# Kernel optimization log

Hardware: AMD Instinct MI355X
Metric: run time of the kernel (lower is better)

Reference implementation:

```python
import jax, jax.numpy as jnp
import numpy as np

N = 100000      # number of 1-simplices (edges of the power grid)
NNZ = 3200000   # nonzeros in L1_tilde (avg degree 32)
CIN = 128
COUT = 128
BN_EPS = 1e-5


def setup_inputs() -> dict:
    key = jax.random.key(0)
    ks = jax.random.split(key, 8)
    Z_H = jax.random.normal(ks[0], (N, CIN), dtype=jnp.float32)
    rows = jax.random.randint(ks[1], (NNZ,), 0, N)
    cols = jax.random.randint(ks[2], (NNZ,), 0, N)
    values = jax.random.normal(ks[3], (NNZ,), dtype=jnp.float32)
    # nn.Linear params (Kaiming-ish scale)
    W = jax.random.normal(ks[4], (CIN, COUT), dtype=jnp.float32) / np.float32(np.sqrt(CIN))
    b = jnp.zeros((COUT,), dtype=jnp.float32)
    # BatchNorm1d affine params
    gamma = jnp.ones((COUT,), dtype=jnp.float32)
    beta = jnp.zeros((COUT,), dtype=jnp.float32)
    return {"Z_H": Z_H, "values": values, "W": W, "b": b,
            "gamma": gamma, "beta": beta, "rows": rows, "cols": cols}


def reference(Z_H, values, W, b, gamma, beta, rows, cols):
    # Linear projection: [N, CIN] @ [CIN, COUT] + [COUT]
    Z_theta = Z_H @ W + b
    # Sparse Laplacian matmul (COO SpMM): Z_conv[r] += v * Z_theta[c]
    gathered = values[:, None] * Z_theta[cols]          # [NNZ, COUT]
    Z_conv = jax.ops.segment_sum(gathered, rows, num_segments=Z_H.shape[0])
    # BatchNorm1d (training mode: biased batch stats over the node dim)
    mean = jnp.mean(Z_conv, axis=0)
    var = jnp.var(Z_conv, axis=0)
    Z_bn = (Z_conv - mean) * (gamma / jnp.sqrt(var + BN_EPS)) + beta
    # ReLU + row-wise max pool -> [N, 1]
    Z_psi = jax.nn.relu(Z_bn)
    return jnp.max(Z_psi, axis=1, keepdims=True)
```

## Files before the change

### kernel.cpp

```cpp
#include <hip/hip_runtime.h>
#include <hip/hip_bf16.h>

#define CIN  128
#define COUT 128
#define BN_EPS 1e-5f
#define RPB   64
#define MAXNB 2048
#define PCHUNK 8192
#define CAP   2560
#define LDP   136

typedef __attribute__((ext_vector_type(8))) short short8;
typedef __attribute__((ext_vector_type(4))) float f32x4;

__device__ __forceinline__ unsigned pk2bf(float lo, float hi) {
    union { __hip_bfloat162 h; unsigned u; } c;
    c.h = __float22bfloat162_rn(make_float2(lo, hi));
    return c.u;
}

__device__ __forceinline__ unsigned short f2bf(float f) {
    unsigned u = __float_as_uint(f);
    u += 0x7fffu + ((u >> 16) & 1u);
    return (unsigned short)(u >> 16);
}

__device__ __forceinline__ void gemm_body(
    const float* __restrict__ Z, const float* __restrict__ W,
    const float* __restrict__ b, unsigned short* __restrict__ Zt,
    int N, int bid, int gb)
{
    __shared__ unsigned short cls[64 * LDP];

    const int t    = threadIdx.x;
    const int lane = t & 63;
    const int wid  = t >> 6;
    const int lm   = lane & 15;
    const int lg   = lane >> 4;

    short8 bfr[4][8];
#pragma unroll
    for (int kc = 0; kc < 4; ++kc) {
#pragma unroll
        for (int ct = 0; ct < 8; ++ct) {
            union { short8 v; unsigned u32[4]; } bf;
#pragma unroll
            for (int e = 0; e < 8; e += 2) {
                const float w0 = W[(kc * 32 + lg * 8 + e)     * COUT + ct * 16 + lm];
                const float w1 = W[(kc * 32 + lg * 8 + e + 1) * COUT + ct * 16 + lm];
                bf.u32[e >> 1] = pk2bf(w0, w1);
            }
            bfr[kc][ct] = bf.v;
        }
    }

    float bias[8];
#pragma unroll
    for (int ct = 0; ct < 8; ++ct) bias[ct] = b[ct * 16 + lm];

    const int tr = t >> 4;
    const int cc = t & 15;

    const int ntiles = (N + 63) / 64;
    for (int tile = bid; tile < ntiles; tile += gb) {
        const int row0 = tile * 64 + wid * 16;
        const int arow = row0 + lm;
        const bool aval = arow < N;
        const float* zrow = Z + (size_t)arow * CIN;

        f32x4 acc[8];
#pragma unroll
        for (int ct = 0; ct < 8; ++ct) {
            f32x4 a = {bias[ct], bias[ct], bias[ct], bias[ct]};
            acc[ct] = a;
        }

#pragma unroll
        for (int kc = 0; kc < 4; ++kc) {
            union { short8 v; unsigned u32[4]; } af;
            if (aval) {
                const float4 z0 = *((const float4*)(zrow + kc * 32 + lg * 8));
                const float4 z1 = *((const float4*)(zrow + kc * 32 + lg * 8 + 4));
                af.u32[0] = pk2bf(z0.x, z0.y);
                af.u32[1] = pk2bf(z0.z, z0.w);
                af.u32[2] = pk2bf(z1.x, z1.y);
                af.u32[3] = pk2bf(z1.z, z1.w);
            } else {
#pragma unroll
                for (int e = 0; e < 4; ++e) af.u32[e] = 0;
            }
#pragma unroll
            for (int ct = 0; ct < 8; ++ct)
                acc[ct] = __builtin_amdgcn_mfma_f32_16x16x32_bf16(
                    af.v, bfr[kc][ct], acc[ct], 0, 0, 0);
        }

        __syncthreads();
#pragma unroll
        for (int i = 0; i < 4; ++i) {
            const int r = wid * 16 + lg * 4 + i;
#pragma unroll
            for (int ct = 0; ct < 8; ct += 2) {
                const unsigned u = pk2bf(acc[ct][i], acc[ct + 1][i]);
                cls[r * LDP + ct * 16 + lm]       = (unsigned short)(u & 0xffffu);
                cls[r * LDP + (ct + 1) * 16 + lm] = (unsigned short)(u >> 16);
            }
        }
        __syncthreads();

#pragma unroll
        for (int j = 0; j < 4; ++j) {
            const int r = j * 16 + tr;
            const int grow = tile * 64 + r;
            if (grow < N) {
                const uint4 v = *((const uint4*)&cls[r * LDP + cc * 8]);
                *((uint4*)(Zt + (size_t)grow * COUT + cc * 8)) = v;
            }
        }
    }
}

__device__ __forceinline__ void partition_body(
    const int* __restrict__ rows, const int* __restrict__ cols,
    const float* __restrict__ vals, int* __restrict__ bucketCur,
    uint2* __restrict__ ebuck, int nnz, int NB, int pb)
{
    __shared__ int h[MAXNB];
    __shared__ int basecur[MAXNB];
    const int t = threadIdx.x;

    for (int i = t; i < NB; i += 256) h[i] = 0;
    __syncthreads();

    const int c0 = pb * PCHUNK;
    const int ce = min(c0 + PCHUNK, nnz);

    int rloc[PCHUNK / 256];
#pragma unroll
    for (int j = 0; j < PCHUNK / 256; ++j) {
        const int i = c0 + j * 256 + t;
        int r = -1;
        if (i < ce) r = rows[i];
        rloc[j] = r;
        if (r >= 0) atomicAdd(&h[r >> 6], 1);
    }
    __syncthreads();

    for (int i = t; i < NB; i += 256) {
        const int c = h[i];
        basecur[i] = c ? (i * CAP + atomicAdd(&bucketCur[i], c)) : 0;
    }
    __syncthreads();

#pragma unroll
    for (int j = 0; j < PCHUNK / 256; ++j) {
        const int i = c0 + j * 256 + t;
        const int r = rloc[j];
        if (r >= 0) {
            const int p = atomicAdd(&basecur[r >> 6], 1);
            ebuck[p] = make_uint2((unsigned)cols[i] | ((unsigned)(r & (RPB - 1)) << 17),
                                  __float_as_uint(vals[i]));
        }
    }
}

__global__ __launch_bounds__(256, 2) void gemm_part_kernel(
    const float* __restrict__ Z, const float* __restrict__ W,
    const float* __restrict__ b, unsigned short* __restrict__ Zt,
    const int* __restrict__ rows, const int* __restrict__ cols,
    const float* __restrict__ vals, int* __restrict__ bucketCur,
    uint2* __restrict__ ebuck, int nnz, int N, int NB, int pblocks, int gb)
{
    if ((int)blockIdx.x < pblocks) {
        partition_body(rows, cols, vals, bucketCur, ebuck, nnz, NB, blockIdx.x);
    } else {
        gemm_body(Z, W, b, Zt, N, blockIdx.x - pblocks, gb);
    }
}

__global__ __launch_bounds__(256) void gather_build_kernel(
    const unsigned short* __restrict__ Zt, const uint2* __restrict__ ebuck,
    const int* __restrict__ bucketCur, unsigned int* __restrict__ Zc,
    float* __restrict__ stats, int N)
{
    __shared__ int cnt[RPB];
    __shared__ int scn[RPB];
    __shared__ int loc[RPB];
    __shared__ uint2 ebuf[CAP];
    __shared__ float sbuf[256];

    const int t = threadIdx.x;
    const int b = blockIdx.x;
    const int base = b * CAP;
    int count = bucketCur[b];
    if (count > CAP) count = CAP;

    sbuf[t] = 0.f;
    if (t < RPB) cnt[t] = 0;
    __syncthreads();

    uint2 er[CAP / 256];
#pragma unroll
    for (int j = 0; j < CAP / 256; ++j) {
        const int i = j * 256 + t;
        if (i < count) {
            er[j] = ebuck[base + i];
            atomicAdd(&cnt[er[j].x >> 17], 1);
        }
    }
    __syncthreads();

    if (t < RPB) scn[t] = cnt[t];
    __syncthreads();
#pragma unroll
    for (int off = 1; off < RPB; off <<= 1) {
        int v = 0;
        if (t < RPB && t >= off) v = scn[t - off];
        __syncthreads();
        if (t < RPB) scn[t] += v;
        __syncthreads();
    }
    if (t < RPB) loc[t] = scn[t] - cnt[t];
    __syncthreads();

#pragma unroll
    for (int j = 0; j < CAP / 256; ++j) {
        const int i = j * 256 + t;
        if (i < count) {
            const uint2 e = er[j];
            const int rl  = (int)(e.x >> 17);
            const int pos = atomicAdd(&loc[rl], 1);
            ebuf[pos] = make_uint2(e.x & 0x1FFFFu, e.y);
        }
    }
    __syncthreads();

    const int wid  = t >> 6;
    const int lane = t & 63;
    const int eo   = lane >> 5;
    const int cg   = lane & 31;

    float s0 = 0.f, s1 = 0.f, s2 = 0.f, s3 = 0.f;
    float q0 = 0.f, q1 = 0.f, q2 = 0.f, q3 = 0.f;

    const int row0 = b * RPB;
    for (int r = wid; r < RPB; r += 4) {
        const int row = row0 + r;
        if (row >= N) break;
        const int end = scn[r];
        const int beg = end - cnt[r];

        float a0 = 0.f, a1 = 0.f, a2 = 0.f, a3 = 0.f;

        int i = beg + eo;
        for (; i + 6 < end; i += 8) {
            const uint2 p0 = ebuf[i];
            const uint2 p1 = ebuf[i + 2];
            const uint2 p2 = ebuf[i + 4];
            const uint2 p3 = ebuf[i + 6];
            const uint2 g0 = *((const uint2*)(Zt + (size_t)p0.x * COUT + cg * 4));
            const uint2 g1 = *((const uint2*)(Zt + (size_t)p1.x * COUT + cg * 4));
            const uint2 g2 = *((const uint2*)(Zt + (size_t)p2.x * COUT + cg * 4));
            const uint2 g3 = *((const uint2*)(Zt + (size_t)p3.x * COUT + cg * 4));
            const float v0 = __uint_as_float(p0.y);
            const float v1 = __uint_as_float(p1.y);
            const float v2 = __uint_as_float(p2.y);
            const float v3 = __uint_as_float(p3.y);
            a0 = fmaf(v0, __uint_as_float(g0.x << 16), a0);
            a1 = fmaf(v0, __uint_as_float(g0.x & 0xffff0000u), a1);
            a2 = fmaf(v0, __uint_as_float(g0.y << 16), a2);
            a3 = fmaf(v0, __uint_as_float(g0.y & 0xffff0000u), a3);
            a0 = fmaf(v1, __uint_as_float(g1.x << 16), a0);
            a1 = fmaf(v1, __uint_as_float(g1.x & 0xffff0000u), a1);
            a2 = fmaf(v1, __uint_as_float(g1.y << 16), a2);
            a3 = fmaf(v1, __uint_as_float(g1.y & 0xffff0000u), a3);
            a0 = fmaf(v2, __uint_as_float(g2.x << 16), a0);
            a1 = fmaf(v2, __uint_as_float(g2.x & 0xffff0000u), a1);
            a2 = fmaf(v2, __uint_as_float(g2.y << 16), a2);
            a3 = fmaf(v2, __uint_as_float(g2.y & 0xffff0000u), a3);
            a0 = fmaf(v3, __uint_as_float(g3.x << 16), a0);
            a1 = fmaf(v3, __uint_as_float(g3.x & 0xffff0000u), a1);
            a2 = fmaf(v3, __uint_as_float(g3.y << 16), a2);
            a3 = fmaf(v3, __uint_as_float(g3.y & 0xffff0000u), a3);
        }
        for (; i < end; i += 2) {
            const uint2 p = ebuf[i];
            const uint2 g = *((const uint2*)(Zt + (size_t)p.x * COUT + cg * 4));
            const float vp = __uint_as_float(p.y);
            a0 = fmaf(vp, __uint_as_float(g.x << 16), a0);
            a1 = fmaf(vp, __uint_as_float(g.x & 0xffff0000u), a1);
            a2 = fmaf(vp, __uint_as_float(g.y << 16), a2);
            a3 = fmaf(vp, __uint_as_float(g.y & 0xffff0000u), a3);
        }

        a0 += __shfl_xor(a0, 32);
        a1 += __shfl_xor(a1, 32);
        a2 += __shfl_xor(a2, 32);
        a3 += __shfl_xor(a3, 32);

        if (eo == 0) {
            uint2 o;
            o.x = pk2bf(a0, a1);
            o.y = pk2bf(a2, a3);
            *((uint2*)(Zc + (size_t)row * (COUT / 2) + cg * 2)) = o;
            s0 += a0; s1 += a1; s2 += a2; s3 += a3;
            q0 = fmaf(a0, a0, q0);
            q1 = fmaf(a1, a1, q1);
            q2 = fmaf(a2, a2, q2);
            q3 = fmaf(a3, a3, q3);
        }
    }

    if (eo == 0) {
        const int c0 = cg * 4;
        atomicAdd(&sbuf[c0 + 0], s0);
        atomicAdd(&sbuf[c0 + 1], s1);
        atomicAdd(&sbuf[c0 + 2], s2);
        atomicAdd(&sbuf[c0 + 3], s3);
        atomicAdd(&sbuf[128 + c0 + 0], q0);
        atomicAdd(&sbuf[128 + c0 + 1], q1);
        atomicAdd(&sbuf[128 + c0 + 2], q2);
        atomicAdd(&sbuf[128 + c0 + 3], q3);
    }
    __syncthreads();
    atomicAdd(&stats[t], sbuf[t]);
}

__global__ __launch_bounds__(256) void finalize_kernel(
    const unsigned int* __restrict__ Zc, const float* __restrict__ stats,
    const float* __restrict__ gamma, const float* __restrict__ beta,
    float* __restrict__ out, int N)
{
    const int row = blockIdx.x * 4 + (threadIdx.x >> 6);
    if (row >= N) return;
    const int lane = threadIdx.x & 63;
    const int c0 = lane * 2;

    const unsigned g = Zc[(size_t)row * (COUT / 2) + lane];
    const float x0 = __uint_as_float(g << 16);
    const float x1 = __uint_as_float(g & 0xffff0000u);

    const float invN = 1.0f / (float)N;
    const float m0 = stats[c0] * invN;
    const float m1 = stats[c0 + 1] * invN;
    const float v0 = stats[128 + c0] * invN - m0 * m0;
    const float v1 = stats[128 + c0 + 1] * invN - m1 * m1;
    const float sc0 = gamma[c0]     * rsqrtf(v0 + BN_EPS);
    const float sc1 = gamma[c0 + 1] * rsqrtf(v1 + BN_EPS);

    float y0 = (x0 - m0) * sc0 + beta[c0];
    float y1 = (x1 - m1) * sc1 + beta[c0 + 1];
    y0 = fmaxf(y0, 0.f);
    y1 = fmaxf(y1, 0.f);

    float mx = fmaxf(y0, y1);
#pragma unroll
    for (int off = 32; off > 0; off >>= 1)
        mx = fmaxf(mx, __shfl_xor(mx, off));

    if (lane == 0) out[row] = mx;
}

extern "C" void kernel_launch(void* const* d_in, const int* in_sizes, int n_in,
                              void* d_out, int out_size, void* d_ws, size_t ws_size,
                              hipStream_t stream)
{
    const float* Z_H   = (const float*)d_in[0];
    const float* vals  = (const float*)d_in[1];
    const float* W     = (const float*)d_in[2];
    const float* b     = (const float*)d_in[3];
    const float* gamma = (const float*)d_in[4];
    const float* beta  = (const float*)d_in[5];
    const int*   rows  = (const int*)d_in[6];
    const int*   cols  = (const int*)d_in[7];
    float* out = (float*)d_out;

    const int N   = in_sizes[0] / CIN;
    const int nnz = in_sizes[1];
    const int NB  = (N + RPB - 1) / RPB;
    const int pblocks = (nnz + PCHUNK - 1) / PCHUNK;
    const int ntiles  = (N + 63) / 64;
    const int gb      = (ntiles + 2) / 3;

    char* ws = (char*)d_ws;
    size_t off = 0;
    unsigned short* Zt = (unsigned short*)(ws + off); off += (size_t)N * COUT * sizeof(unsigned short);
    unsigned int*   Zc = (unsigned int*)(ws + off);   off += (size_t)N * (COUT / 2) * sizeof(unsigned int);
    uint2* ebuck  = (uint2*)(ws + off);  off += (size_t)NB * CAP * sizeof(uint2);
    int* bucketCur = (int*)(ws + off);   off += (size_t)NB * sizeof(int);
    float* stats   = (float*)(ws + off); off += 256 * sizeof(float);

    hipMemsetAsync(bucketCur, 0, ((size_t)NB + 256) * sizeof(int), stream);

    gemm_part_kernel<<<pblocks + gb, 256, 0, stream>>>(
        Z_H, W, b, Zt, rows, cols, vals, bucketCur, ebuck, nnz, N, NB, pblocks, gb);

    gather_build_kernel<<<NB, 256, 0, stream>>>(Zt, ebuck, bucketCur, Zc, stats, N);

    finalize_kernel<<<(N + 3) / 4, 256, 0, stream>>>(Zc, stats, gamma, beta, out, N);
}
```

Before: 242.9 us.

## Split SpMM gather into two 64-channel passes to halve per-pass row footprint

The SpMM aggregation loop now runs twice per block, each pass gathering only 64 of the 128 bf16 channels (4-byte loads instead of 8-byte) and writing half of each output row. Each pass touches a smaller slice of the gathered Z_theta rows, which may improve cache hit rates for the random gathers. In exchange, the edge list in shared memory is walked twice, the number of gather instructions doubles, and each load is narrower. The unused f2bf helper is also removed.

```diff
diff --git a/kernel.cpp b/kernel.cpp
--- a/kernel.cpp
+++ b/kernel.cpp
@@ -17,12 +17,6 @@
     union { __hip_bfloat162 h; unsigned u; } c;
     c.h = __float22bfloat162_rn(make_float2(lo, hi));
     return c.u;
-}
-
-__device__ __forceinline__ unsigned short f2bf(float f) {
-    unsigned u = __float_as_uint(f);
-    u += 0x7fffu + ((u >> 16) & 1u);
-    return (unsigned short)(u >> 16);
 }
 
 __device__ __forceinline__ void gemm_body(
@@ -240,87 +234,70 @@
     const int eo   = lane >> 5;
     const int cg   = lane & 31;
 
-    float s0 = 0.f, s1 = 0.f, s2 = 0.f, s3 = 0.f;
-    float q0 = 0.f, q1 = 0.f, q2 = 0.f, q3 = 0.f;
-
     const int row0 = b * RPB;
-    for (int r = wid; r < RPB; r += 4) {
-        const int row = row0 + r;
-        if (row >= N) break;
-        const int end = scn[r];
-        const int beg = end - cnt[r];
-
-        float a0 = 0.f, a1 = 0.f, a2 = 0.f, a3 = 0.f;
-
-        int i = beg + eo;
-        for (; i + 6 < end; i += 8) {
-            const uint2 p0 = ebuf[i];
-            const uint2 p1 = ebuf[i + 2];
-            const uint2 p2 = ebuf[i + 4];
-            const uint2 p3 = ebuf[i + 6];
-            const uint2 g0 = *((const uint2*)(Zt + (size_t)p0.x * COUT + cg * 4));
-            const uint2 g1 = *((const uint2*)(Zt + (size_t)p1.x * COUT + cg * 4));
-            const uint2 g2 = *((const uint2*)(Zt + (size_t)p2.x * COUT + cg * 4));
-            const uint2 g3 = *((const uint2*)(Zt + (size_t)p3.x * COUT + cg * 4));
-            const float v0 = __uint_as_float(p0.y);
-            const float v1 = __uint_as_float(p1.y);
-            const float v2 = __uint_as_float(p2.y);
-            const float v3 = __uint_as_float(p3.y);
-            a0 = fmaf(v0, __uint_as_float(g0.x << 16), a0);
-            a1 = fmaf(v0, __uint_as_float(g0.x & 0xffff0000u), a1);
-            a2 = fmaf(v0, __uint_as_float(g0.y << 16), a2);
-            a3 = fmaf(v0, __uint_as_float(g0.y & 0xffff0000u), a3);
-            a0 = fmaf(v1, __uint_as_float(g1.x << 16), a0);
-            a1 = fmaf(v1, __uint_as_float(g1.x & 0xffff0000u), a1);
-            a2 = fmaf(v1, __uint_as_float(g1.y << 16), a2);
-            a3 = fmaf(v1, __uint_as_float(g1.y & 0xffff0000u), a3);
-            a0 = fmaf(v2, __uint_as_float(g2.x << 16), a0);
-            a1 = fmaf(v2, __uint_as_float(g2.x & 0xffff0000u), a1);
-            a2 = fmaf(v2, __uint_as_float(g2.y << 16), a2);
-            a3 = fmaf(v2, __uint_as_float(g2.y & 0xffff0000u), a3);
-            a0 = fmaf(v3, __uint_as_float(g3.x << 16), a0);
-            a1 = fmaf(v3, __uint_as_float(g3.x & 0xffff0000u), a1);
-            a2 = fmaf(v3, __uint_as_float(g3.y << 16), a2);
-            a3 = fmaf(v3, __uint_as_float(g3.y & 0xffff0000u), a3);
-        }
-        for (; i < end; i += 2) {
-            const uint2 p = ebuf[i];
-            const uint2 g = *((const uint2*)(Zt + (size_t)p.x * COUT + cg * 4));
-            const float vp = __uint_as_float(p.y);
-            a0 = fmaf(vp, __uint_as_float(g.x << 16), a0);
-            a1 = fmaf(vp, __uint_as_float(g.x & 0xffff0000u), a1);
-            a2 = fmaf(vp, __uint_as_float(g.y << 16), a2);
-            a3 = fmaf(vp, __uint_as_float(g.y & 0xffff0000u), a3);
-        }
-
-        a0 += __shfl_xor(a0, 32);
-        a1 += __shfl_xor(a1, 32);
-        a2 += __shfl_xor(a2, 32);
-        a3 += __shfl_xor(a3, 32);
+
+#pragma unroll
+    for (int pass = 0; pass < 2; ++pass) {
+        const int choff = pass * 64 + cg * 2;
+
+        float s0 = 0.f, s1 = 0.f, q0 = 0.f, q1 = 0.f;
+
+        for (int r = wid; r < RPB; r += 4) {
+            const int row = row0 + r;
+            if (row >= N) break;
+            const int end = scn[r];
+            const int beg = end - cnt[r];
+
+            float a0 = 0.f, a1 = 0.f;
+
+            int i = beg + eo;
+            for (; i + 6 < end; i += 8) {
+                const uint2 p0 = ebuf[i];
+                const uint2 p1 = ebuf[i + 2];
+                const uint2 p2 = ebuf[i + 4];
+                const uint2 p3 = ebuf[i + 6];
+                const unsigned g0 = *((const unsigned*)(Zt + (size_t)p0.x * COUT + choff));
+                const unsigned g1 = *((const unsigned*)(Zt + (size_t)p1.x * COUT + choff));
+                const unsigned g2 = *((const unsigned*)(Zt + (size_t)p2.x * COUT + choff));
+                const unsigned g3 = *((const unsigned*)(Zt + (size_t)p3.x * COUT + choff));
+                const float v0 = __uint_as_float(p0.y);
+                const float v1 = __uint_as_float(p1.y);
+                const float v2 = __uint_as_float(p2.y);
+                const float v3 = __uint_as_float(p3.y);
+                a0 = fmaf(v0, __uint_as_float(g0 << 16), a0);
+                a1 = fmaf(v0, __uint_as_float(g0 & 0xffff0000u), a1);
+                a0 = fmaf(v1, __uint_as_float(g1 << 16), a0);
+                a1 = fmaf(v1, __uint_as_float(g1 & 0xffff0000u), a1);
+                a0 = fmaf(v2, __uint_as_float(g2 << 16), a0);
+                a1 = fmaf(v2, __uint_as_float(g2 & 0xffff0000u), a1);
+                a0 = fmaf(v3, __uint_as_float(g3 << 16), a0);
+                a1 = fmaf(v3, __uint_as_float(g3 & 0xffff0000u), a1);
+            }
+            for (; i < end; i += 2) {
+                const uint2 p = ebuf[i];
+                const unsigned g = *((const unsigned*)(Zt + (size_t)p.x * COUT + choff));
+                const float vp = __uint_as_float(p.y);
+                a0 = fmaf(vp, __uint_as_float(g << 16), a0);
+                a1 = fmaf(vp, __uint_as_float(g & 0xffff0000u), a1);
+            }
+
+            a0 += __shfl_xor(a0, 32);
+            a1 += __shfl_xor(a1, 32);
+
+            if (eo == 0) {
+                Zc[(size_t)row * (COUT / 2) + pass * 32 + cg] = pk2bf(a0, a1);
+                s0 += a0; s1 += a1;
+                q0 = fmaf(a0, a0, q0);
+                q1 = fmaf(a1, a1, q1);
+            }
+        }
 
         if (eo == 0) {
-            uint2 o;
-            o.x = pk2bf(a0, a1);
-            o.y = pk2bf(a2, a3);
-            *((uint2*)(Zc + (size_t)row * (COUT / 2) + cg * 2)) = o;
-            s0 += a0; s1 += a1; s2 += a2; s3 += a3;
-            q0 = fmaf(a0, a0, q0);
-            q1 = fmaf(a1, a1, q1);
-            q2 = fmaf(a2, a2, q2);
-            q3 = fmaf(a3, a3, q3);
-        }
-    }
-
-    if (eo == 0) {
-        const int c0 = cg * 4;
-        atomicAdd(&sbuf[c0 + 0], s0);
-        atomicAdd(&sbuf[c0 + 1], s1);
-        atomicAdd(&sbuf[c0 + 2], s2);
-        atomicAdd(&sbuf[c0 + 3], s3);
-        atomicAdd(&sbuf[128 + c0 + 0], q0);
-        atomicAdd(&sbuf[128 + c0 + 1], q1);
-        atomicAdd(&sbuf[128 + c0 + 2], q2);
-        atomicAdd(&sbuf[128 + c0 + 3], q3);
+            atomicAdd(&sbuf[choff + 0], s0);
+            atomicAdd(&sbuf[choff + 1], s1);
+            atomicAdd(&sbuf[128 + choff + 0], q0);
+            atomicAdd(&sbuf[128 + choff + 1], q1);
+        }
     }
     __syncthreads();
     atomicAdd(&stats[t], sbuf[t]);
```

After: 232.7 us. -4.2%, faster.
